# Performance work log

Hardware: AMD Instinct MI355X
Metric: run time of the kernel (lower is better)

Reference implementation:

```python
import jax, jax.numpy as jnp
import numpy as np

NUM_HEADS = 8

def setup_inputs() -> dict:
    key = jax.random.key(0)
    ks = jax.random.split(key, 12)
    B, C, H, W = 4, 256, 64, 64
    QK = 256
    NSP = 256
    x = jax.random.normal(ks[0], (B, C, H, W), dtype=jnp.float32)
    affinity_matrix = jax.random.uniform(ks[1], (B, NSP, H * W), dtype=jnp.float32)
    norm_w = 1.0 + 0.02 * jax.random.normal(ks[2], (C,), dtype=jnp.float32)
    norm_b = 0.02 * jax.random.normal(ks[3], (C,), dtype=jnp.float32)
    Wq = 0.02 * jax.random.normal(ks[4], (QK, C), dtype=jnp.float32)
    Wk = 0.02 * jax.random.normal(ks[5], (QK, C), dtype=jnp.float32)
    Wv = 0.02 * jax.random.normal(ks[6], (C, C), dtype=jnp.float32)
    Wsp = 0.02 * jax.random.normal(ks[7], (QK, C), dtype=jnp.float32)
    lepe_w = 0.02 * jax.random.normal(ks[8], (C, 1, 3, 3), dtype=jnp.float32)  # depthwise OIHW
    lepe_b = 0.02 * jax.random.normal(ks[9], (C,), dtype=jnp.float32)
    return {"x": x, "affinity_matrix": affinity_matrix, "norm_w": norm_w,
            "norm_b": norm_b, "Wq": Wq, "Wk": Wk, "Wv": Wv, "Wsp": Wsp,
            "lepe_w": lepe_w, "lepe_b": lepe_b, "num_spixels": NSP}


def _layernorm2d(x, w, b, eps=1e-6):
    # LayerNorm over channel dim of NCHW input
    xp = x.transpose(0, 2, 3, 1)  # B,H,W,C
    mu = xp.mean(-1, keepdims=True)
    var = ((xp - mu) ** 2).mean(-1, keepdims=True)
    xn = (xp - mu) * jax.lax.rsqrt(var + eps) * w + b
    return xn.transpose(0, 3, 1, 2)


def _sgca(x, affinity_matrix, norm_w, norm_b, Wq, Wk, Wv, Wsp, lepe_w, lepe_b, num_spixels):
    B, C, H, W = x.shape
    HW = H * W
    h = NUM_HEADS
    qk_dim = Wq.shape[0]
    dqk = qk_dim // h
    dv = C // h
    scale = (C // h) ** -0.5

    xn = _layernorm2d(x, norm_w, norm_b)

    # superpixel aggregation: b (hw) c
    x_flat = xn.reshape(B, C, HW).transpose(0, 2, 1)  # B,HW,C
    stoken = jnp.einsum('bmn,bnc->bmc', affinity_matrix, x_flat)
    stoken = stoken / (affinity_matrix.sum(-1, keepdims=True) + 1e-16)  # B,nsp,C

    # sp projection -> B,h,dqk,nsp
    st = jnp.einsum('bmc,qc->bmq', stoken, Wsp).transpose(0, 2, 1)
    st = st.reshape(B, h, dqk, num_spixels)

    # 1x1 conv projections
    q = jnp.einsum('oc,bchw->bohw', Wq, xn).reshape(B, h, dqk, HW)
    k = jnp.einsum('oc,bchw->bohw', Wk, xn).reshape(B, h, dqk, HW)
    vx = jnp.einsum('oc,bchw->bohw', Wv, xn)  # B,C,H,W
    v = vx.reshape(B, h, dv, HW)

    # LePE: depthwise 3x3 conv on v(x)
    lepe = jax.lax.conv_general_dilated(
        vx, lepe_w, window_strides=(1, 1), padding=((1, 1), (1, 1)),
        feature_group_count=C, dimension_numbers=('NCHW', 'OIHW', 'NCHW'))
    lepe = lepe + lepe_b[None, :, None, None]
    # faithful to original: [B,C,HW] -> permute -> [B,HW,C] -> reshape B,C,H,W
    lepe = lepe.reshape(B, C, HW).transpose(0, 2, 1).reshape(B, C, H, W)

    # stage 1: k^T @ stoken, softmax over HW axis
    s_attn = jnp.einsum('bhdn,bhdm->bhnm', k, st) * scale  # B,h,HW,nsp
    s_attn = jax.nn.softmax(s_attn, axis=-2)
    s_out = jnp.einsum('bhdn,bhnm->bhdm', v, s_attn)  # B,h,dv,nsp

    # stage 2: stoken^T @ q, softmax over nsp axis
    x_attn = jnp.einsum('bhdm,bhdn->bhmn', st, q) * scale  # B,h,nsp,HW
    x_attn = jax.nn.softmax(x_attn, axis=-2)
    x_out = jnp.einsum('bhdm,bhmn->bhdn', s_out, x_attn).reshape(B, C, H, W)

    return x_out + lepe


def reference(x, affinity_matrix, norm_w, norm_b, Wq, Wk, Wv, Wsp, lepe_w, lepe_b, num_spixels):
    return _sgca(x, affinity_matrix, norm_w, norm_b, Wq, Wk, Wv, Wsp, lepe_w, lepe_b, num_spixels)
```

## Files before the change

kernel.cpp:

```cpp
#include <hip/hip_runtime.h>
#include <hip/hip_bf16.h>

#define BATCH 4
#define CCH   256
#define HWHW  4096
#define NSP   256
#define NHEAD 8
#define SCALE 0.17677669529663689f
#define PLANE 1048576L

typedef short bf16x8 __attribute__((ext_vector_type(8)));
typedef float f32x4  __attribute__((ext_vector_type(4)));

__global__ __launch_bounds__(256)
void ln_fused_kernel(const float* __restrict__ x, const float* __restrict__ w,
                     const float* __restrict__ bb,
                     const float* __restrict__ Wq, const float* __restrict__ Wk,
                     const float* __restrict__ Wv, const float* __restrict__ Wsp,
                     __hip_bfloat16* __restrict__ xn_cn,
                     __hip_bfloat16* __restrict__ xn_nc,
                     __hip_bfloat16* __restrict__ wbf)
{
    __shared__ __hip_bfloat16 xs[256][80];
    __shared__ float ps[16][64], pss[16][64];
    __shared__ float mus[64], rstds[64];
    __shared__ float wls[256], bls[256];
    int blk = blockIdx.x;
    int t = threadIdx.x;
    if (blk >= 256) {
        int sel = blk - 256;
        const float* src = (sel == 0) ? Wq : (sel == 1) ? Wk : (sel == 2) ? Wv : Wsp;
        __hip_bfloat16* dst = wbf + sel * 65536;
        for (int i = t * 4; i < 65536; i += 1024) {
            float4 f = *(const float4*)(src + i);
            __hip_bfloat16 p[4];
            p[0] = __float2bfloat16(f.x); p[1] = __float2bfloat16(f.y);
            p[2] = __float2bfloat16(f.z); p[3] = __float2bfloat16(f.w);
            *(int2*)(dst + i) = *(int2*)p;
        }
        return;
    }
    int b = blk >> 6;
    int n0 = (blk & 63) * 64;
    int px4 = t & 15, cg = t >> 4;
    wls[t] = w[t]; bls[t] = bb[t];
    long base = (long)b * CCH * HWHW + n0 + px4 * 4;
    float s0 = 0.f, s1 = 0.f, s2 = 0.f, s3 = 0.f;
    float q0 = 0.f, q1 = 0.f, q2 = 0.f, q3 = 0.f;
#pragma unroll
    for (int j = 0; j < 16; ++j) {
        int c = cg * 16 + j;
        float4 f = *(const float4*)(x + base + (long)c * HWHW);
        s0 += f.x; s1 += f.y; s2 += f.z; s3 += f.w;
        q0 += f.x * f.x; q1 += f.y * f.y; q2 += f.z * f.z; q3 += f.w * f.w;
        __hip_bfloat16 p[4];
        p[0] = __float2bfloat16(f.x); p[1] = __float2bfloat16(f.y);
        p[2] = __float2bfloat16(f.z); p[3] = __float2bfloat16(f.w);
        *(int2*)&xs[c][px4 * 4] = *(int2*)p;
    }
    *(float4*)&ps[cg][px4 * 4]  = float4{s0, s1, s2, s3};
    *(float4*)&pss[cg][px4 * 4] = float4{q0, q1, q2, q3};
    __syncthreads();
    if (t < 64) {
        float S = 0.f, SS = 0.f;
#pragma unroll
        for (int g = 0; g < 16; ++g) { S += ps[g][t]; SS += pss[g][t]; }
        float mu = S * (1.f / 256.f);
        float var = SS * (1.f / 256.f) - mu * mu;
        mus[t] = mu; rstds[t] = rsqrtf(var + 1e-6f);
    }
    __syncthreads();
    float mu[4], rst[4];
#pragma unroll
    for (int i = 0; i < 4; ++i) { mu[i] = mus[px4 * 4 + i]; rst[i] = rstds[px4 * 4 + i]; }
#pragma unroll
    for (int j = 0; j < 16; ++j) {
        int c = cg * 16 + j;
        __hip_bfloat16 p[4];
        *(int2*)p = *(const int2*)&xs[c][px4 * 4];
        float wc = wls[c], bc = bls[c];
#pragma unroll
        for (int i = 0; i < 4; ++i)
            p[i] = __float2bfloat16(((float)p[i] - mu[i]) * rst[i] * wc + bc);
        *(int2*)&xs[c][px4 * 4] = *(int2*)p;
    }
    __syncthreads();
#pragma unroll
    for (int i = 0; i < 8; ++i) {
        int idx = t + i * 256;
        int c = idx >> 3, seg = idx & 7;
        *(int4*)(xn_cn + (long)(b * CCH + c) * HWHW + n0 + seg * 8) =
            *(const int4*)&xs[c][seg * 8];
    }
#pragma unroll
    for (int i = 0; i < 8; ++i) {
        int idx = t + i * 256;
        int px = idx >> 5, g8 = idx & 31;
        short pack[8];
#pragma unroll
        for (int j = 0; j < 8; ++j) {
            __hip_bfloat16 v = xs[g8 * 8 + j][px];
            pack[j] = *(short*)&v;
        }
        *(int4*)(xn_nc + ((long)b * HWHW + n0 + px) * CCH + g8 * 8) = *(int4*)pack;
    }
}

__global__ __launch_bounds__(256)
void reduce8_cast_kernel(const float* __restrict__ part, const float* __restrict__ rsPart,
                         __hip_bfloat16* __restrict__ out, float* __restrict__ rs)
{
    int i = blockIdx.x * 256 + threadIdx.x;
    if (blockIdx.x < 4) {
        int b = i >> 8, m = i & 255;
        float s = 0.f;
#pragma unroll
        for (int ch = 0; ch < 8; ++ch) s += rsPart[((b * 8 + ch) << 8) + m];
        rs[i] = s;
    }
    int b = i >> 16, idx = i & 65535;
    long base = (long)b * 8 * 65536 + idx;
    float s = 0.f;
#pragma unroll
    for (int ch = 0; ch < 8; ++ch) s += part[base + (long)ch * 65536];
    out[i] = __float2bfloat16(s);
}

template <int OUTK, bool ROWSCALE, bool A32, bool ROWSUM>
__global__ __launch_bounds__(256)
void mfma_gemm_nt(const void* __restrict__ Aptr, const __hip_bfloat16* __restrict__ B,
                  void* __restrict__ Cptr, int N, int K, int kChunk, int kShift,
                  long aStrideZ, long bStrideZ, long cStrideZ,
                  const float* __restrict__ rowScale, long sStrideZ,
                  float* __restrict__ rsPart)
{
    __shared__ __hip_bfloat16 Asm[4 * 64 * 8];
    __shared__ __hip_bfloat16 Bsm[4 * 64 * 8];
    int z = blockIdx.z;
    int b = z >> kShift;
    int ch = z & ((1 << kShift) - 1);
    int t = threadIdx.x;
    int lane = t & 63, w = t >> 6;
    int l15 = lane & 15, quad = lane >> 4;
    int Mt = blockIdx.y * 64, Nt = blockIdx.x * 64;

    const float* aSrcF = A32 ? ((const float*)Aptr + b * aStrideZ + (long)ch * kChunk
                                + (long)(Mt + w * 16 + l15) * K + quad * 8) : nullptr;
    const __hip_bfloat16* aSrcB = A32 ? nullptr :
        ((const __hip_bfloat16*)Aptr + b * aStrideZ + (long)ch * kChunk
         + (long)(Mt + w * 16 + l15) * K + quad * 8);
    const __hip_bfloat16* bSrc = B + b * bStrideZ + (long)ch * kChunk
        + (long)(Nt + w * 16 + l15) * K + quad * 8;
    __hip_bfloat16* aDst = &Asm[t * 8];
    __hip_bfloat16* bDst = &Bsm[t * 8];

    f32x4 acc00 = {0.f,0.f,0.f,0.f}, acc01 = acc00, acc10 = acc00, acc11 = acc00;
    f32x4 rs0 = acc00, rs1 = acc00;
    bf16x8 onesf;
    { short o = (l15 == 0) ? (short)0x3F80 : (short)0;
      onesf = bf16x8{o, o, o, o, o, o, o, o}; }
    int wm = (w & 1) * 2, wn = (w >> 1) * 2;

    float4 aF0, aF1; int4 aReg, bReg;
    if (A32) { aF0 = ((const float4*)aSrcF)[0]; aF1 = ((const float4*)aSrcF)[1]; }
    else aReg = *(const int4*)aSrcB;
    bReg = *(const int4*)bSrc;

    for (int k0 = 0; k0 < kChunk; k0 += 32) {
        if (A32) {
            __hip_bfloat16 tmp[8];
            tmp[0]=__float2bfloat16(aF0.x); tmp[1]=__float2bfloat16(aF0.y);
            tmp[2]=__float2bfloat16(aF0.z); tmp[3]=__float2bfloat16(aF0.w);
            tmp[4]=__float2bfloat16(aF1.x); tmp[5]=__float2bfloat16(aF1.y);
            tmp[6]=__float2bfloat16(aF1.z); tmp[7]=__float2bfloat16(aF1.w);
            *(int4*)aDst = *(const int4*)tmp;
        } else {
            *(int4*)aDst = aReg;
        }
        *(int4*)bDst = bReg;
        __syncthreads();
        if (k0 + 32 < kChunk) {
            bSrc += 32;
            if (A32) { aSrcF += 32; aF0 = ((const float4*)aSrcF)[0]; aF1 = ((const float4*)aSrcF)[1]; }
            else     { aSrcB += 32; aReg = *(const int4*)aSrcB; }
            bReg = *(const int4*)bSrc;
        }
        bf16x8 a0 = ((const bf16x8*)Asm)[wm * 64 + lane];
        bf16x8 a1 = ((const bf16x8*)Asm)[(wm + 1) * 64 + lane];
        bf16x8 b0 = ((const bf16x8*)Bsm)[wn * 64 + lane];
        bf16x8 b1 = ((const bf16x8*)Bsm)[(wn + 1) * 64 + lane];
        acc00 = __builtin_amdgcn_mfma_f32_16x16x32_bf16(a0, b0, acc00, 0, 0, 0);
        acc01 = __builtin_amdgcn_mfma_f32_16x16x32_bf16(a0, b1, acc01, 0, 0, 0);
        acc10 = __builtin_amdgcn_mfma_f32_16x16x32_bf16(a1, b0, acc10, 0, 0, 0);
        acc11 = __builtin_amdgcn_mfma_f32_16x16x32_bf16(a1, b1, acc11, 0, 0, 0);
        if (ROWSUM) {
            rs0 = __builtin_amdgcn_mfma_f32_16x16x32_bf16(a0, onesf, rs0, 0, 0, 0);
            rs1 = __builtin_amdgcn_mfma_f32_16x16x32_bf16(a1, onesf, rs1, 0, 0, 0);
        }
        __syncthreads();
    }
    if (ROWSUM && blockIdx.x == 0 && (w >> 1) == 0 && l15 == 0) {
#pragma unroll
        for (int r = 0; r < 4; ++r) {
            rsPart[(long)z * 256 + Mt + wm * 16 + quad * 4 + r]       = rs0[r];
            rsPart[(long)z * 256 + Mt + (wm + 1) * 16 + quad * 4 + r] = rs1[r];
        }
    }
    f32x4 accs[2][2] = {{acc00, acc01}, {acc10, acc11}};
#pragma unroll
    for (int i = 0; i < 2; ++i)
#pragma unroll
        for (int j = 0; j < 2; ++j)
#pragma unroll
            for (int r = 0; r < 4; ++r) {
                int m = Mt + (wm + i) * 16 + quad * 4 + r;
                int n = Nt + (wn + j) * 16 + l15;
                float val = accs[i][j][r];
                if (ROWSCALE) val /= (rowScale[(long)b * sStrideZ + m] + 1e-16f);
                long off = (long)z * cStrideZ + (long)m * N + n;
                if (OUTK == 0) ((float*)Cptr)[off] = val;
                else ((__hip_bfloat16*)Cptr)[off] = __float2bfloat16(val);
            }
}

__global__ __launch_bounds__(256)
void stage1_mfma(const __hip_bfloat16* __restrict__ qk_nc,
                 const __hip_bfloat16* __restrict__ v_cn,
                 const __hip_bfloat16* __restrict__ st_md,
                 __hip_bfloat16* __restrict__ opart)
{
    __shared__ __hip_bfloat16 Es[256 * 72];
    __shared__ __hip_bfloat16 sts[256 * 40];
    const int chunk = blockIdx.x, bh = blockIdx.y;
    const int b = bh >> 3, h = bh & 7;
    const int t = threadIdx.x, lane = t & 63, w = t >> 6;
    const int l15 = lane & 15, quad = lane >> 4;
    const int n0 = chunk * 256;

    {
        const int4* src = (const int4*)(st_md + ((long)(b * 256 + t)) * 256 + h * 32);
        int4* dst = (int4*)&sts[t * 40];
        dst[0] = src[0]; dst[1] = src[1]; dst[2] = src[2]; dst[3] = src[3];
    }
    __syncthreads();
    bf16x8 afrag[16];
#pragma unroll
    for (int mt = 0; mt < 16; ++mt)
        afrag[mt] = *(const bf16x8*)&sts[(mt * 16 + l15) * 40 + quad * 8];
    bf16x8 onesf;
    { short o = (l15 == 0) ? (short)0x3F80 : (short)0;
      onesf = bf16x8{o, o, o, o, o, o, o, o}; }

    f32x4 occ[4][3];
#pragma unroll
    for (int i = 0; i < 4; ++i)
#pragma unroll
        for (int j = 0; j < 3; ++j) occ[i][j] = f32x4{0.f,0.f,0.f,0.f};

    for (int sub = 0; sub < 4; ++sub) {
        const int nbase = n0 + sub * 64;
        bf16x8 kf = *(const bf16x8*)(qk_nc + ((long)b * 4096 + nbase + 16 * w + l15) * 512 + 256 + h * 32 + quad * 8);
#pragma unroll
        for (int mt = 0; mt < 16; ++mt) {
            f32x4 s = __builtin_amdgcn_mfma_f32_16x16x32_bf16(afrag[mt], kf, f32x4{0.f,0.f,0.f,0.f}, 0, 0, 0);
#pragma unroll
            for (int r = 0; r < 4; ++r)
                Es[(mt * 16 + quad * 4 + r) * 72 + 16 * w + l15] =
                    __float2bfloat16(__expf(s[r] * SCALE));
        }
        __syncthreads();
#pragma unroll
        for (int ks = 0; ks < 2; ++ks) {
            bf16x8 bf0 = *(const bf16x8*)(v_cn + ((long)(b * 256 + h * 32 + l15)) * 4096 + nbase + ks * 32 + quad * 8);
            bf16x8 bf1 = *(const bf16x8*)(v_cn + ((long)(b * 256 + h * 32 + 16 + l15)) * 4096 + nbase + ks * 32 + quad * 8);
#pragma unroll
            for (int mi = 0; mi < 4; ++mi) {
                bf16x8 af = *(const bf16x8*)&Es[(64 * w + mi * 16 + l15) * 72 + ks * 32 + quad * 8];
                occ[mi][0] = __builtin_amdgcn_mfma_f32_16x16x32_bf16(af, bf0, occ[mi][0], 0, 0, 0);
                occ[mi][1] = __builtin_amdgcn_mfma_f32_16x16x32_bf16(af, bf1, occ[mi][1], 0, 0, 0);
                occ[mi][2] = __builtin_amdgcn_mfma_f32_16x16x32_bf16(af, onesf, occ[mi][2], 0, 0, 0);
            }
        }
        __syncthreads();
    }
    __hip_bfloat16* tb = Es;
#pragma unroll
    for (int mi = 0; mi < 4; ++mi)
#pragma unroll
        for (int jt = 0; jt < 3; ++jt) {
            if (jt == 2 && l15 != 0) continue;
            int col = jt * 16 + l15;
#pragma unroll
            for (int r = 0; r < 4; ++r) {
                int m = 64 * w + mi * 16 + quad * 4 + r;
                tb[col * 264 + m] = __float2bfloat16(occ[mi][jt][r]);
            }
        }
    __syncthreads();
    int* og = (int*)(opart) + (long)(chunk * 32 + bh) * 4224;
    const int* tbi = (const int*)tb;
#pragma unroll
    for (int i = 0; i < 17; ++i) {
        int idx = t + i * 256;
        if (idx < 4224) {
            int row = idx >> 7, off = idx & 127;
            og[idx] = tbi[row * 132 + off];
        }
    }
}

__global__ __launch_bounds__(256)
void merge1_kernel(const __hip_bfloat16* __restrict__ opart, __hip_bfloat16* __restrict__ sout)
{
    int t = blockIdx.x * 256 + threadIdx.x;
    int m = t & 255;
    int d = (t >> 8) & 31;
    int bh = t >> 13;
    float num = 0.f, den = 0.f;
    for (int ch = 0; ch < 16; ++ch) {
        long base = (long)((ch * 32 + bh) * 33) * 256 + m;
        num += (float)opart[base + (long)d * 256];
        den += (float)opart[base + 32 * 256];
    }
    sout[(long)bh * 8192 + d * 256 + m] = __float2bfloat16(num / den);
}

__global__ __launch_bounds__(256)
void lepe_conv_t_kernel(const __hip_bfloat16* __restrict__ v_cn,
                        const float* __restrict__ lw, const float* __restrict__ lb,
                        __hip_bfloat16* __restrict__ lepe_cn)
{
    __shared__ __hip_bfloat16 in_t[32 * 384];
    __shared__ __hip_bfloat16 tile_bf[256 * 33];
    __shared__ float wls[288], bls[32];
    const int bx = blockIdx.x;
    const int c0 = blockIdx.y * 32;
    const int b  = blockIdx.z;
    const int t = threadIdx.x;
    const int n0 = bx * 256, r0 = bx * 4;

    for (int i = t; i < 288; i += 256) wls[i] = lw[c0 * 9 + i];
    if (t < 32)  bls[t] = lb[c0 + t];
#pragma unroll
    for (int i = 0; i < 6; ++i) {
        int vi = t + i * 256;
        int ch = vi / 48;
        int off = (vi % 48) * 8;
        int g = (r0 - 1) * 64 + off;
        int4 val = {0, 0, 0, 0};
        if ((unsigned)g < 4096u)
            val = *(const int4*)(v_cn + (((long)(b * CCH + c0 + ch)) << 12) + g);
        *(int4*)&in_t[ch * 384 + off] = val;
    }
    __syncthreads();

    const int lane = t & 63, w = t >> 6;
#pragma unroll
    for (int i = 0; i < 8; ++i) {
        int ch = w * 8 + i;
        float cr[6], lf[6], rf[6];
#pragma unroll
        for (int rr = 0; rr < 6; ++rr) {
            cr[rr] = (float)in_t[ch * 384 + rr * 64 + lane];
            float lv = __shfl_up(cr[rr], 1);
            float rv = __shfl_down(cr[rr], 1);
            lf[rr] = (lane == 0) ? 0.f : lv;
            rf[rr] = (lane == 63) ? 0.f : rv;
        }
        float w0 = wls[ch*9+0], w1 = wls[ch*9+1], w2 = wls[ch*9+2];
        float w3 = wls[ch*9+3], w4 = wls[ch*9+4], w5 = wls[ch*9+5];
        float w6 = wls[ch*9+6], w7 = wls[ch*9+7], w8 = wls[ch*9+8];
        float bias = bls[ch];
#pragma unroll
        for (int r = 0; r < 4; ++r) {
            float acc = bias
                + lf[r]   * w0 + cr[r]   * w1 + rf[r]   * w2
                + lf[r+1] * w3 + cr[r+1] * w4 + rf[r+1] * w5
                + lf[r+2] * w6 + cr[r+2] * w7 + rf[r+2] * w8;
            tile_bf[(r * 64 + lane) * 33 + ch] = __float2bfloat16(acc);
        }
    }
    __syncthreads();
#pragma unroll
    for (int i = 0; i < 32; ++i) {
        int idx = t + i * 256;
        int nl = idx >> 5, cj = idx & 31;
        int sp = n0 + nl;
        lepe_cn[((long)(b * CCH + (sp >> 4)) << 12) + (nl & 15) * 256 + c0 + cj] =
            tile_bf[nl * 33 + cj];
    }
}

__global__ __launch_bounds__(256)
void stage2_mfma(const __hip_bfloat16* __restrict__ qk_nc,
                 const __hip_bfloat16* __restrict__ st_md,
                 const __hip_bfloat16* __restrict__ sout_bf,
                 const __hip_bfloat16* __restrict__ lepe_cn,
                 float* __restrict__ out)
{
    __shared__ __hip_bfloat16 Es2[64 * 264];
    __shared__ __hip_bfloat16 sts[256 * 40];
    __shared__ __hip_bfloat16 sos[32 * 264];
    __shared__ float o_t[32 * 68];
    const int chunk = blockIdx.x, bh = blockIdx.y;
    const int b = bh >> 3, h = bh & 7;
    const int t = threadIdx.x, lane = t & 63, w = t >> 6;
    const int l15 = lane & 15, quad = lane >> 4;
    const int n0 = chunk * 256;

    {
        const int4* src = (const int4*)(st_md + ((long)(b * 256 + t)) * 256 + h * 32);
        int4* dst = (int4*)&sts[t * 40];
        dst[0] = src[0]; dst[1] = src[1]; dst[2] = src[2]; dst[3] = src[3];
    }
    {
        int row = t >> 3, seg = t & 7;
        const int4* src = (const int4*)(sout_bf + (long)bh * 8192 + row * 256 + seg * 32);
        int4* dst = (int4*)&sos[row * 264 + seg * 32];
        dst[0] = src[0]; dst[1] = src[1]; dst[2] = src[2]; dst[3] = src[3];
    }
    __syncthreads();
    bf16x8 stfrag[4];
#pragma unroll
    for (int mt = 0; mt < 4; ++mt)
        stfrag[mt] = *(const bf16x8*)&sts[(64 * w + mt * 16 + l15) * 40 + quad * 8];
    bf16x8 onesf;
    { short o = (l15 == 0) ? (short)0x3F80 : (short)0;
      onesf = bf16x8{o, o, o, o, o, o, o, o}; }

    for (int sub = 0; sub < 4; ++sub) {
        const int nbase = n0 + sub * 64;
#pragma unroll
        for (int nt = 0; nt < 4; ++nt) {
            bf16x8 qf = *(const bf16x8*)(qk_nc + ((long)b * 4096 + nbase + nt * 16 + l15) * 512 + h * 32 + quad * 8);
#pragma unroll
            for (int mt = 0; mt < 4; ++mt) {
                f32x4 s = __builtin_amdgcn_mfma_f32_16x16x32_bf16(qf, stfrag[mt], f32x4{0.f,0.f,0.f,0.f}, 0, 0, 0);
#pragma unroll
                for (int r = 0; r < 4; ++r)
                    Es2[(nt * 16 + quad * 4 + r) * 264 + 64 * w + mt * 16 + l15] =
                        __float2bfloat16(__expf(s[r] * SCALE));
            }
        }
        __syncthreads();
        f32x4 o0 = {0.f,0.f,0.f,0.f}, o1 = o0, o2 = o0;
#pragma unroll
        for (int ks = 0; ks < 8; ++ks) {
            bf16x8 af = *(const bf16x8*)&Es2[(16 * w + l15) * 264 + ks * 32 + quad * 8];
            bf16x8 b0 = *(const bf16x8*)&sos[(l15) * 264 + ks * 32 + quad * 8];
            bf16x8 b1 = *(const bf16x8*)&sos[(16 + l15) * 264 + ks * 32 + quad * 8];
            o0 = __builtin_amdgcn_mfma_f32_16x16x32_bf16(af, b0, o0, 0, 0, 0);
            o1 = __builtin_amdgcn_mfma_f32_16x16x32_bf16(af, b1, o1, 0, 0, 0);
            o2 = __builtin_amdgcn_mfma_f32_16x16x32_bf16(af, onesf, o2, 0, 0, 0);
        }
        __syncthreads();
#pragma unroll
        for (int r = 0; r < 4; ++r) {
            float den = __shfl(o2[r], lane & 48);
            float inv = 1.f / den;
            o_t[(l15) * 68 + 16 * w + quad * 4 + r]      = o0[r] * inv;
            o_t[(16 + l15) * 68 + 16 * w + quad * 4 + r] = o1[r] * inv;
        }
        __syncthreads();
        {
            int row = t >> 3, coff = (t & 7) * 8;
            long gb = ((long)(b * 256 + h * 32 + row)) * 4096 + nbase + coff;
            int4 lp4 = *(const int4*)(lepe_cn + gb);
            const __hip_bfloat16* lp = (const __hip_bfloat16*)&lp4;
            const float* sp = &o_t[row * 68 + coff];
            float4 r0, r1;
            r0.x = sp[0] + (float)lp[0]; r0.y = sp[1] + (float)lp[1];
            r0.z = sp[2] + (float)lp[2]; r0.w = sp[3] + (float)lp[3];
            r1.x = sp[4] + (float)lp[4]; r1.y = sp[5] + (float)lp[5];
            r1.z = sp[6] + (float)lp[6]; r1.w = sp[7] + (float)lp[7];
            *(float4*)(out + gb)     = r0;
            *(float4*)(out + gb + 4) = r1;
        }
        __syncthreads();
    }
}

extern "C" void kernel_launch(void* const* d_in, const int* in_sizes, int n_in,
                              void* d_out, int out_size, void* d_ws, size_t ws_size,
                              hipStream_t stream)
{
    const float* x    = (const float*)d_in[0];
    const float* aff  = (const float*)d_in[1];
    const float* nw   = (const float*)d_in[2];
    const float* nb   = (const float*)d_in[3];
    const float* Wq   = (const float*)d_in[4];
    const float* Wk   = (const float*)d_in[5];
    const float* Wv   = (const float*)d_in[6];
    const float* Wsp  = (const float*)d_in[7];
    const float* lw   = (const float*)d_in[8];
    const float* lb   = (const float*)d_in[9];
    float* out = (float*)d_out;

    float* ws = (float*)d_ws;
    const long P = PLANE;
    __hip_bfloat16* qk_nc  = (__hip_bfloat16*)(ws);
    __hip_bfloat16* v_cn   = (__hip_bfloat16*)(ws + 4 * P);
    __hip_bfloat16* xn_cn  = (__hip_bfloat16*)(ws + 6 * P);
    __hip_bfloat16* xn_nc  = (__hip_bfloat16*)(ws + 8 * P);
    __hip_bfloat16* lepe_cn= (__hip_bfloat16*)(ws + 10 * P);
    float* stoken_part = ws + 12 * P;
    __hip_bfloat16* opart = (__hip_bfloat16*)(ws + 14 * P);
    float* tail        = ws + 14 * P + 2162688;
    __hip_bfloat16* wbf       = (__hip_bfloat16*)tail;
    __hip_bfloat16* stoken_bf = (__hip_bfloat16*)(tail + 131072);
    __hip_bfloat16* st_md     = (__hip_bfloat16*)(tail + 262144);
    __hip_bfloat16* sout_bf   = (__hip_bfloat16*)(tail + 393216);
    float* rs      = tail + 524288;
    float* rs_part = tail + 525312;

    ln_fused_kernel<<<260, 256, 0, stream>>>(x, nw, nb, Wq, Wk, Wv, Wsp,
                                             xn_cn, xn_nc, wbf);
    mfma_gemm_nt<0, false, true, true><<<dim3(4, 4, 32), 256, 0, stream>>>(
        aff, xn_cn, stoken_part, 256, 4096, 512, 3, P, P, 65536L, nullptr, 0, rs_part);
    reduce8_cast_kernel<<<1024, 256, 0, stream>>>(stoken_part, rs_part, stoken_bf, rs);
    mfma_gemm_nt<1, true, false, false><<<dim3(4, 4, 4), 256, 0, stream>>>(
        stoken_bf, wbf + 3 * 65536, st_md, 256, 256, 256, 0, 65536L, 0L, 65536L, rs, 256L, nullptr);
    mfma_gemm_nt<1, false, false, false><<<dim3(8, 64, 4), 256, 0, stream>>>(
        xn_nc, wbf, qk_nc, 512, 256, 256, 0, P, 0L, 2 * P, nullptr, 0, nullptr);
    mfma_gemm_nt<1, false, false, false><<<dim3(64, 4, 4), 256, 0, stream>>>(
        wbf + 2 * 65536, xn_nc, v_cn, 4096, 256, 256, 0, 0L, P, P, nullptr, 0, nullptr);
    lepe_conv_t_kernel<<<dim3(16, 8, BATCH), 256, 0, stream>>>(v_cn, lw, lb, lepe_cn);
    stage1_mfma<<<dim3(16, 32), 256, 0, stream>>>(qk_nc, v_cn, st_md, opart);
    merge1_kernel<<<1024, 256, 0, stream>>>(opart, sout_bf);
    stage2_mfma<<<dim3(16, 32), 256, 0, stream>>>(qk_nc, st_md, sout_bf, lepe_cn, out);
}
```

Measured before the change: 217.6 us.

## Merge independent GEMMs and LePE conv into fewer grouped kernel launches

Drops the separate split-K reduction kernel by folding the 8-way partial-sum reduction and row normalisation into the stoken projection GEMM. That GEMM is combined with the Q/K and V projection GEMMs into one grouped launch that branches on block index. The LePE depthwise conv is merged into the stage-1 attention kernel as extra blocks. This cuts launch count and inter-kernel gaps, at the cost of redundant reads of partials and rowsum recomputation per output element, and larger shared memory per block in the merged stage-1 kernel.

```diff
diff --git a/kernel.cpp b/kernel.cpp
--- a/kernel.cpp
+++ b/kernel.cpp
@@ -107,50 +107,22 @@
 }
 
 __global__ __launch_bounds__(256)
-void reduce8_cast_kernel(const float* __restrict__ part, const float* __restrict__ rsPart,
-                         __hip_bfloat16* __restrict__ out, float* __restrict__ rs)
-{
-    int i = blockIdx.x * 256 + threadIdx.x;
-    if (blockIdx.x < 4) {
-        int b = i >> 8, m = i & 255;
-        float s = 0.f;
-#pragma unroll
-        for (int ch = 0; ch < 8; ++ch) s += rsPart[((b * 8 + ch) << 8) + m];
-        rs[i] = s;
-    }
-    int b = i >> 16, idx = i & 65535;
-    long base = (long)b * 8 * 65536 + idx;
-    float s = 0.f;
-#pragma unroll
-    for (int ch = 0; ch < 8; ++ch) s += part[base + (long)ch * 65536];
-    out[i] = __float2bfloat16(s);
-}
-
-template <int OUTK, bool ROWSCALE, bool A32, bool ROWSUM>
-__global__ __launch_bounds__(256)
-void mfma_gemm_nt(const void* __restrict__ Aptr, const __hip_bfloat16* __restrict__ B,
-                  void* __restrict__ Cptr, int N, int K, int kChunk, int kShift,
-                  long aStrideZ, long bStrideZ, long cStrideZ,
-                  const float* __restrict__ rowScale, long sStrideZ,
-                  float* __restrict__ rsPart)
+void stoken_gemm_kernel(const float* __restrict__ A, const __hip_bfloat16* __restrict__ B,
+                        float* __restrict__ C, float* __restrict__ rsPart)
 {
     __shared__ __hip_bfloat16 Asm[4 * 64 * 8];
     __shared__ __hip_bfloat16 Bsm[4 * 64 * 8];
     int z = blockIdx.z;
-    int b = z >> kShift;
-    int ch = z & ((1 << kShift) - 1);
+    int b = z >> 3, ch = z & 7;
     int t = threadIdx.x;
     int lane = t & 63, w = t >> 6;
     int l15 = lane & 15, quad = lane >> 4;
     int Mt = blockIdx.y * 64, Nt = blockIdx.x * 64;
 
-    const float* aSrcF = A32 ? ((const float*)Aptr + b * aStrideZ + (long)ch * kChunk
-                                + (long)(Mt + w * 16 + l15) * K + quad * 8) : nullptr;
-    const __hip_bfloat16* aSrcB = A32 ? nullptr :
-        ((const __hip_bfloat16*)Aptr + b * aStrideZ + (long)ch * kChunk
-         + (long)(Mt + w * 16 + l15) * K + quad * 8);
-    const __hip_bfloat16* bSrc = B + b * bStrideZ + (long)ch * kChunk
-        + (long)(Nt + w * 16 + l15) * K + quad * 8;
+    const float* aSrcF = A + (long)b * PLANE + (long)ch * 512
+        + (long)(Mt + w * 16 + l15) * 4096 + quad * 8;
+    const __hip_bfloat16* bSrc = B + (long)b * PLANE + (long)ch * 512
+        + (long)(Nt + w * 16 + l15) * 4096 + quad * 8;
     __hip_bfloat16* aDst = &Asm[t * 8];
     __hip_bfloat16* bDst = &Bsm[t * 8];
 
@@ -161,28 +133,21 @@
       onesf = bf16x8{o, o, o, o, o, o, o, o}; }
     int wm = (w & 1) * 2, wn = (w >> 1) * 2;
 
-    float4 aF0, aF1; int4 aReg, bReg;
-    if (A32) { aF0 = ((const float4*)aSrcF)[0]; aF1 = ((const float4*)aSrcF)[1]; }
-    else aReg = *(const int4*)aSrcB;
-    bReg = *(const int4*)bSrc;
-
-    for (int k0 = 0; k0 < kChunk; k0 += 32) {
-        if (A32) {
-            __hip_bfloat16 tmp[8];
-            tmp[0]=__float2bfloat16(aF0.x); tmp[1]=__float2bfloat16(aF0.y);
-            tmp[2]=__float2bfloat16(aF0.z); tmp[3]=__float2bfloat16(aF0.w);
-            tmp[4]=__float2bfloat16(aF1.x); tmp[5]=__float2bfloat16(aF1.y);
-            tmp[6]=__float2bfloat16(aF1.z); tmp[7]=__float2bfloat16(aF1.w);
-            *(int4*)aDst = *(const int4*)tmp;
-        } else {
-            *(int4*)aDst = aReg;
-        }
+    float4 aF0 = ((const float4*)aSrcF)[0], aF1 = ((const float4*)aSrcF)[1];
+    int4 bReg = *(const int4*)bSrc;
+
+    for (int k0 = 0; k0 < 512; k0 += 32) {
+        __hip_bfloat16 tmp[8];
+        tmp[0]=__float2bfloat16(aF0.x); tmp[1]=__float2bfloat16(aF0.y);
+        tmp[2]=__float2bfloat16(aF0.z); tmp[3]=__float2bfloat16(aF0.w);
+        tmp[4]=__float2bfloat16(aF1.x); tmp[5]=__float2bfloat16(aF1.y);
+        tmp[6]=__float2bfloat16(aF1.z); tmp[7]=__float2bfloat16(aF1.w);
+        *(int4*)aDst = *(const int4*)tmp;
         *(int4*)bDst = bReg;
         __syncthreads();
-        if (k0 + 32 < kChunk) {
-            bSrc += 32;
-            if (A32) { aSrcF += 32; aF0 = ((const float4*)aSrcF)[0]; aF1 = ((const float4*)aSrcF)[1]; }
-            else     { aSrcB += 32; aReg = *(const int4*)aSrcB; }
+        if (k0 + 32 < 512) {
+            aSrcF += 32; bSrc += 32;
+            aF0 = ((const float4*)aSrcF)[0]; aF1 = ((const float4*)aSrcF)[1];
             bReg = *(const int4*)bSrc;
         }
         bf16x8 a0 = ((const bf16x8*)Asm)[wm * 64 + lane];
@@ -193,17 +158,130 @@
         acc01 = __builtin_amdgcn_mfma_f32_16x16x32_bf16(a0, b1, acc01, 0, 0, 0);
         acc10 = __builtin_amdgcn_mfma_f32_16x16x32_bf16(a1, b0, acc10, 0, 0, 0);
         acc11 = __builtin_amdgcn_mfma_f32_16x16x32_bf16(a1, b1, acc11, 0, 0, 0);
-        if (ROWSUM) {
-            rs0 = __builtin_amdgcn_mfma_f32_16x16x32_bf16(a0, onesf, rs0, 0, 0, 0);
-            rs1 = __builtin_amdgcn_mfma_f32_16x16x32_bf16(a1, onesf, rs1, 0, 0, 0);
-        }
-        __syncthreads();
-    }
-    if (ROWSUM && blockIdx.x == 0 && (w >> 1) == 0 && l15 == 0) {
+        rs0 = __builtin_amdgcn_mfma_f32_16x16x32_bf16(a0, onesf, rs0, 0, 0, 0);
+        rs1 = __builtin_amdgcn_mfma_f32_16x16x32_bf16(a1, onesf, rs1, 0, 0, 0);
+        __syncthreads();
+    }
+    if (blockIdx.x == 0 && (w >> 1) == 0 && l15 == 0) {
 #pragma unroll
         for (int r = 0; r < 4; ++r) {
             rsPart[(long)z * 256 + Mt + wm * 16 + quad * 4 + r]       = rs0[r];
             rsPart[(long)z * 256 + Mt + (wm + 1) * 16 + quad * 4 + r] = rs1[r];
+        }
+    }
+    f32x4 accs[2][2] = {{acc00, acc01}, {acc10, acc11}};
+#pragma unroll
+    for (int i = 0; i < 2; ++i)
+#pragma unroll
+        for (int j = 0; j < 2; ++j)
+#pragma unroll
+            for (int r = 0; r < 4; ++r) {
+                int m = Mt + (wm + i) * 16 + quad * 4 + r;
+                int n = Nt + (wn + j) * 16 + l15;
+                C[(long)z * 65536 + (long)m * 256 + n] = accs[i][j][r];
+            }
+}
+
+__global__ __launch_bounds__(256)
+void gemm3_kernel(const __hip_bfloat16* __restrict__ xn_nc,
+                  const __hip_bfloat16* __restrict__ wbf,
+                  const float* __restrict__ stoken_part,
+                  const float* __restrict__ rs_part,
+                  __hip_bfloat16* __restrict__ qk_nc,
+                  __hip_bfloat16* __restrict__ v_cn,
+                  __hip_bfloat16* __restrict__ st_md)
+{
+    __shared__ __hip_bfloat16 Asm[4 * 64 * 8];
+    __shared__ __hip_bfloat16 Bsm[4 * 64 * 8];
+    int B = blockIdx.x;
+    int t = threadIdx.x;
+    int lane = t & 63, w = t >> 6;
+    int l15 = lane & 15, quad = lane >> 4;
+
+    const __hip_bfloat16* aB = nullptr;
+    const float* aP = nullptr;
+    const __hip_bfloat16* bB;
+    __hip_bfloat16* C;
+    int N, Mt, Nt, bIdx;
+    bool stPath = false;
+    if (B < 2048) {
+        int xq = B & 7, y = (B >> 3) & 63, b = B >> 9;
+        Mt = y * 64; Nt = xq * 64; N = 512; bIdx = b;
+        aB = xn_nc + (long)b * PLANE;
+        bB = wbf;
+        C = qk_nc + (long)b * 2 * PLANE;
+    } else if (B < 3072) {
+        int B2 = B - 2048;
+        int xq = B2 & 63, y = (B2 >> 6) & 3, b = B2 >> 8;
+        Mt = y * 64; Nt = xq * 64; N = 4096; bIdx = b;
+        aB = wbf + 2 * 65536;
+        bB = xn_nc + (long)b * PLANE;
+        C = v_cn + (long)b * PLANE;
+    } else {
+        int B2 = B - 3072;
+        int xq = B2 & 3, y = (B2 >> 2) & 3, b = B2 >> 4;
+        Mt = y * 64; Nt = xq * 64; N = 256; bIdx = b;
+        stPath = true;
+        aP = stoken_part + (long)b * 8 * 65536;
+        bB = wbf + 3 * 65536;
+        C = st_md + (long)b * 65536;
+    }
+    __hip_bfloat16* aDst = &Asm[t * 8];
+    __hip_bfloat16* bDst = &Bsm[t * 8];
+    const __hip_bfloat16* bSrc = bB + (long)(Nt + w * 16 + l15) * 256 + quad * 8;
+
+    f32x4 acc00 = {0.f,0.f,0.f,0.f}, acc01 = acc00, acc10 = acc00, acc11 = acc00;
+    int wm = (w & 1) * 2, wn = (w >> 1) * 2;
+
+    if (!stPath) {
+        const __hip_bfloat16* aSrc = aB + (long)(Mt + w * 16 + l15) * 256 + quad * 8;
+        int4 aReg = *(const int4*)aSrc;
+        int4 bReg = *(const int4*)bSrc;
+        for (int k0 = 0; k0 < 256; k0 += 32) {
+            *(int4*)aDst = aReg;
+            *(int4*)bDst = bReg;
+            __syncthreads();
+            if (k0 + 32 < 256) {
+                aSrc += 32; bSrc += 32;
+                aReg = *(const int4*)aSrc; bReg = *(const int4*)bSrc;
+            }
+            bf16x8 a0 = ((const bf16x8*)Asm)[wm * 64 + lane];
+            bf16x8 a1 = ((const bf16x8*)Asm)[(wm + 1) * 64 + lane];
+            bf16x8 b0 = ((const bf16x8*)Bsm)[wn * 64 + lane];
+            bf16x8 b1 = ((const bf16x8*)Bsm)[(wn + 1) * 64 + lane];
+            acc00 = __builtin_amdgcn_mfma_f32_16x16x32_bf16(a0, b0, acc00, 0, 0, 0);
+            acc01 = __builtin_amdgcn_mfma_f32_16x16x32_bf16(a0, b1, acc01, 0, 0, 0);
+            acc10 = __builtin_amdgcn_mfma_f32_16x16x32_bf16(a1, b0, acc10, 0, 0, 0);
+            acc11 = __builtin_amdgcn_mfma_f32_16x16x32_bf16(a1, b1, acc11, 0, 0, 0);
+            __syncthreads();
+        }
+    } else {
+        const float* aPSrc = aP + (long)(Mt + w * 16 + l15) * 256 + quad * 8;
+        for (int k0 = 0; k0 < 256; k0 += 32) {
+            const float* ap = aPSrc + k0;
+            float a8[8] = {0,0,0,0,0,0,0,0};
+#pragma unroll
+            for (int chn = 0; chn < 8; ++chn) {
+                const float4* p = (const float4*)(ap + (long)chn * 65536);
+                float4 f0 = p[0], f1 = p[1];
+                a8[0] += f0.x; a8[1] += f0.y; a8[2] += f0.z; a8[3] += f0.w;
+                a8[4] += f1.x; a8[5] += f1.y; a8[6] += f1.z; a8[7] += f1.w;
+            }
+            __hip_bfloat16 tmp[8];
+#pragma unroll
+            for (int j = 0; j < 8; ++j) tmp[j] = __float2bfloat16(a8[j]);
+            *(int4*)aDst = *(const int4*)tmp;
+            *(int4*)bDst = *(const int4*)(bSrc + k0);
+            __syncthreads();
+            bf16x8 a0 = ((const bf16x8*)Asm)[wm * 64 + lane];
+            bf16x8 a1 = ((const bf16x8*)Asm)[(wm + 1) * 64 + lane];
+            bf16x8 b0 = ((const bf16x8*)Bsm)[wn * 64 + lane];
+            bf16x8 b1 = ((const bf16x8*)Bsm)[(wn + 1) * 64 + lane];
+            acc00 = __builtin_amdgcn_mfma_f32_16x16x32_bf16(a0, b0, acc00, 0, 0, 0);
+            acc01 = __builtin_amdgcn_mfma_f32_16x16x32_bf16(a0, b1, acc01, 0, 0, 0);
+            acc10 = __builtin_amdgcn_mfma_f32_16x16x32_bf16(a1, b0, acc10, 0, 0, 0);
+            acc11 = __builtin_amdgcn_mfma_f32_16x16x32_bf16(a1, b1, acc11, 0, 0, 0);
+            __syncthreads();
         }
     }
     f32x4 accs[2][2] = {{acc00, acc01}, {acc10, acc11}};
@@ -216,95 +294,162 @@
                 int m = Mt + (wm + i) * 16 + quad * 4 + r;
                 int n = Nt + (wn + j) * 16 + l15;
                 float val = accs[i][j][r];
-                if (ROWSCALE) val /= (rowScale[(long)b * sStrideZ + m] + 1e-16f);
-                long off = (long)z * cStrideZ + (long)m * N + n;
-                if (OUTK == 0) ((float*)Cptr)[off] = val;
-                else ((__hip_bfloat16*)Cptr)[off] = __float2bfloat16(val);
+                if (stPath) {
+                    float rsv = 0.f;
+#pragma unroll
+                    for (int chn = 0; chn < 8; ++chn)
+                        rsv += rs_part[((bIdx * 8 + chn) << 8) + m];
+                    val /= (rsv + 1e-16f);
+                }
+                C[(long)m * N + n] = __float2bfloat16(val);
             }
 }
 
 __global__ __launch_bounds__(256)
-void stage1_mfma(const __hip_bfloat16* __restrict__ qk_nc,
-                 const __hip_bfloat16* __restrict__ v_cn,
-                 const __hip_bfloat16* __restrict__ st_md,
-                 __hip_bfloat16* __restrict__ opart)
+void stage1_lepe_kernel(const __hip_bfloat16* __restrict__ qk_nc,
+                        const __hip_bfloat16* __restrict__ v_cn,
+                        const __hip_bfloat16* __restrict__ st_md,
+                        const float* __restrict__ lw, const float* __restrict__ lb,
+                        __hip_bfloat16* __restrict__ opart,
+                        __hip_bfloat16* __restrict__ lepe_cn)
 {
-    __shared__ __hip_bfloat16 Es[256 * 72];
-    __shared__ __hip_bfloat16 sts[256 * 40];
-    const int chunk = blockIdx.x, bh = blockIdx.y;
-    const int b = bh >> 3, h = bh & 7;
-    const int t = threadIdx.x, lane = t & 63, w = t >> 6;
-    const int l15 = lane & 15, quad = lane >> 4;
-    const int n0 = chunk * 256;
-
-    {
-        const int4* src = (const int4*)(st_md + ((long)(b * 256 + t)) * 256 + h * 32);
-        int4* dst = (int4*)&sts[t * 40];
-        dst[0] = src[0]; dst[1] = src[1]; dst[2] = src[2]; dst[3] = src[3];
-    }
-    __syncthreads();
-    bf16x8 afrag[16];
-#pragma unroll
-    for (int mt = 0; mt < 16; ++mt)
-        afrag[mt] = *(const bf16x8*)&sts[(mt * 16 + l15) * 40 + quad * 8];
-    bf16x8 onesf;
-    { short o = (l15 == 0) ? (short)0x3F80 : (short)0;
-      onesf = bf16x8{o, o, o, o, o, o, o, o}; }
-
-    f32x4 occ[4][3];
-#pragma unroll
-    for (int i = 0; i < 4; ++i)
-#pragma unroll
-        for (int j = 0; j < 3; ++j) occ[i][j] = f32x4{0.f,0.f,0.f,0.f};
-
-    for (int sub = 0; sub < 4; ++sub) {
-        const int nbase = n0 + sub * 64;
-        bf16x8 kf = *(const bf16x8*)(qk_nc + ((long)b * 4096 + nbase + 16 * w + l15) * 512 + 256 + h * 32 + quad * 8);
-#pragma unroll
-        for (int mt = 0; mt < 16; ++mt) {
-            f32x4 s = __builtin_amdgcn_mfma_f32_16x16x32_bf16(afrag[mt], kf, f32x4{0.f,0.f,0.f,0.f}, 0, 0, 0);
-#pragma unroll
-            for (int r = 0; r < 4; ++r)
-                Es[(mt * 16 + quad * 4 + r) * 72 + 16 * w + l15] =
-                    __float2bfloat16(__expf(s[r] * SCALE));
-        }
-        __syncthreads();
-#pragma unroll
-        for (int ks = 0; ks < 2; ++ks) {
-            bf16x8 bf0 = *(const bf16x8*)(v_cn + ((long)(b * 256 + h * 32 + l15)) * 4096 + nbase + ks * 32 + quad * 8);
-            bf16x8 bf1 = *(const bf16x8*)(v_cn + ((long)(b * 256 + h * 32 + 16 + l15)) * 4096 + nbase + ks * 32 + quad * 8);
-#pragma unroll
-            for (int mi = 0; mi < 4; ++mi) {
-                bf16x8 af = *(const bf16x8*)&Es[(64 * w + mi * 16 + l15) * 72 + ks * 32 + quad * 8];
-                occ[mi][0] = __builtin_amdgcn_mfma_f32_16x16x32_bf16(af, bf0, occ[mi][0], 0, 0, 0);
-                occ[mi][1] = __builtin_amdgcn_mfma_f32_16x16x32_bf16(af, bf1, occ[mi][1], 0, 0, 0);
-                occ[mi][2] = __builtin_amdgcn_mfma_f32_16x16x32_bf16(af, onesf, occ[mi][2], 0, 0, 0);
-            }
-        }
-        __syncthreads();
-    }
-    __hip_bfloat16* tb = Es;
-#pragma unroll
-    for (int mi = 0; mi < 4; ++mi)
-#pragma unroll
-        for (int jt = 0; jt < 3; ++jt) {
-            if (jt == 2 && l15 != 0) continue;
-            int col = jt * 16 + l15;
+    __shared__ __align__(16) char smem[57344];
+    const int B = blockIdx.x;
+    const int t = threadIdx.x;
+    if (B < 512) {
+        __hip_bfloat16* Es  = (__hip_bfloat16*)smem;
+        __hip_bfloat16* sts = (__hip_bfloat16*)(smem + 36864);
+        const int chunk = B & 15, bh = B >> 4;
+        const int b = bh >> 3, h = bh & 7;
+        const int lane = t & 63, w = t >> 6;
+        const int l15 = lane & 15, quad = lane >> 4;
+        const int n0 = chunk * 256;
+        {
+            const int4* src = (const int4*)(st_md + ((long)(b * 256 + t)) * 256 + h * 32);
+            int4* dst = (int4*)&sts[t * 40];
+            dst[0] = src[0]; dst[1] = src[1]; dst[2] = src[2]; dst[3] = src[3];
+        }
+        __syncthreads();
+        bf16x8 afrag[16];
+#pragma unroll
+        for (int mt = 0; mt < 16; ++mt)
+            afrag[mt] = *(const bf16x8*)&sts[(mt * 16 + l15) * 40 + quad * 8];
+        bf16x8 onesf;
+        { short o = (l15 == 0) ? (short)0x3F80 : (short)0;
+          onesf = bf16x8{o, o, o, o, o, o, o, o}; }
+        f32x4 occ[4][3];
+#pragma unroll
+        for (int i = 0; i < 4; ++i)
+#pragma unroll
+            for (int j = 0; j < 3; ++j) occ[i][j] = f32x4{0.f,0.f,0.f,0.f};
+        for (int sub = 0; sub < 4; ++sub) {
+            const int nbase = n0 + sub * 64;
+            bf16x8 kf = *(const bf16x8*)(qk_nc + ((long)b * 4096 + nbase + 16 * w + l15) * 512 + 256 + h * 32 + quad * 8);
+#pragma unroll
+            for (int mt = 0; mt < 16; ++mt) {
+                f32x4 s = __builtin_amdgcn_mfma_f32_16x16x32_bf16(afrag[mt], kf, f32x4{0.f,0.f,0.f,0.f}, 0, 0, 0);
+#pragma unroll
+                for (int r = 0; r < 4; ++r)
+                    Es[(mt * 16 + quad * 4 + r) * 72 + 16 * w + l15] =
+                        __float2bfloat16(__expf(s[r] * SCALE));
+            }
+            __syncthreads();
+#pragma unroll
+            for (int ks = 0; ks < 2; ++ks) {
+                bf16x8 bf0 = *(const bf16x8*)(v_cn + ((long)(b * 256 + h * 32 + l15)) * 4096 + nbase + ks * 32 + quad * 8);
+                bf16x8 bf1 = *(const bf16x8*)(v_cn + ((long)(b * 256 + h * 32 + 16 + l15)) * 4096 + nbase + ks * 32 + quad * 8);
+#pragma unroll
+                for (int mi = 0; mi < 4; ++mi) {
+                    bf16x8 af = *(const bf16x8*)&Es[(64 * w + mi * 16 + l15) * 72 + ks * 32 + quad * 8];
+                    occ[mi][0] = __builtin_amdgcn_mfma_f32_16x16x32_bf16(af, bf0, occ[mi][0], 0, 0, 0);
+                    occ[mi][1] = __builtin_amdgcn_mfma_f32_16x16x32_bf16(af, bf1, occ[mi][1], 0, 0, 0);
+                    occ[mi][2] = __builtin_amdgcn_mfma_f32_16x16x32_bf16(af, onesf, occ[mi][2], 0, 0, 0);
+                }
+            }
+            __syncthreads();
+        }
+        __hip_bfloat16* tb = Es;
+#pragma unroll
+        for (int mi = 0; mi < 4; ++mi)
+#pragma unroll
+            for (int jt = 0; jt < 3; ++jt) {
+                if (jt == 2 && l15 != 0) continue;
+                int col = jt * 16 + l15;
+#pragma unroll
+                for (int r = 0; r < 4; ++r) {
+                    int m = 64 * w + mi * 16 + quad * 4 + r;
+                    tb[col * 264 + m] = __float2bfloat16(occ[mi][jt][r]);
+                }
+            }
+        __syncthreads();
+        int* og = (int*)(opart) + (long)(chunk * 32 + bh) * 4224;
+        const int* tbi = (const int*)tb;
+#pragma unroll
+        for (int i = 0; i < 17; ++i) {
+            int idx = t + i * 256;
+            if (idx < 4224) {
+                int row = idx >> 7, off = idx & 127;
+                og[idx] = tbi[row * 132 + off];
+            }
+        }
+    } else {
+        __hip_bfloat16* in_t    = (__hip_bfloat16*)smem;
+        __hip_bfloat16* tile_bf = (__hip_bfloat16*)(smem + 24576);
+        float* wls = (float*)(smem + 41472);
+        float* bls = (float*)(smem + 42624);
+        int B2 = B - 512;
+        const int bx = B2 & 15;
+        const int c0 = ((B2 >> 4) & 7) * 32;
+        const int b  = B2 >> 7;
+        const int n0 = bx * 256, r0 = bx * 4;
+        for (int i = t; i < 288; i += 256) wls[i] = lw[c0 * 9 + i];
+        if (t < 32)  bls[t] = lb[c0 + t];
+#pragma unroll
+        for (int i = 0; i < 6; ++i) {
+            int vi = t + i * 256;
+            int ch = vi / 48;
+            int off = (vi % 48) * 8;
+            int g = (r0 - 1) * 64 + off;
+            int4 val = {0, 0, 0, 0};
+            if ((unsigned)g < 4096u)
+                val = *(const int4*)(v_cn + (((long)(b * CCH + c0 + ch)) << 12) + g);
+            *(int4*)&in_t[ch * 384 + off] = val;
+        }
+        __syncthreads();
+        const int lane = t & 63, w = t >> 6;
+#pragma unroll
+        for (int i = 0; i < 8; ++i) {
+            int ch = w * 8 + i;
+            float cr[6], lf[6], rf[6];
+#pragma unroll
+            for (int rr = 0; rr < 6; ++rr) {
+                cr[rr] = (float)in_t[ch * 384 + rr * 64 + lane];
+                float lv = __shfl_up(cr[rr], 1);
+                float rv = __shfl_down(cr[rr], 1);
+                lf[rr] = (lane == 0) ? 0.f : lv;
+                rf[rr] = (lane == 63) ? 0.f : rv;
+            }
+            float w0 = wls[ch*9+0], w1 = wls[ch*9+1], w2 = wls[ch*9+2];
+            float w3 = wls[ch*9+3], w4 = wls[ch*9+4], w5 = wls[ch*9+5];
+            float w6 = wls[ch*9+6], w7 = wls[ch*9+7], w8 = wls[ch*9+8];
+            float bias = bls[ch];
 #pragma unroll
             for (int r = 0; r < 4; ++r) {
-                int m = 64 * w + mi * 16 + quad * 4 + r;
-                tb[col * 264 + m] = __float2bfloat16(occ[mi][jt][r]);
-            }
-        }
-    __syncthreads();
-    int* og = (int*)(opart) + (long)(chunk * 32 + bh) * 4224;
-    const int* tbi = (const int*)tb;
-#pragma unroll
-    for (int i = 0; i < 17; ++i) {
-        int idx = t + i * 256;
-        if (idx < 4224) {
-            int row = idx >> 7, off = idx & 127;
-            og[idx] = tbi[row * 132 + off];
+                float acc = bias
+                    + lf[r]   * w0 + cr[r]   * w1 + rf[r]   * w2
+                    + lf[r+1] * w3 + cr[r+1] * w4 + rf[r+1] * w5
+                    + lf[r+2] * w6 + cr[r+2] * w7 + rf[r+2] * w8;
+                tile_bf[(r * 64 + lane) * 33 + ch] = __float2bfloat16(acc);
+            }
+        }
+        __syncthreads();
+#pragma unroll
+        for (int i = 0; i < 32; ++i) {
+            int idx = t + i * 256;
+            int nl = idx >> 5, cj = idx & 31;
+            int sp = n0 + nl;
+            lepe_cn[((long)(b * CCH + (sp >> 4)) << 12) + (nl & 15) * 256 + c0 + cj] =
+                tile_bf[nl * 33 + cj];
         }
     }
 }
@@ -323,72 +468,6 @@
         den += (float)opart[base + 32 * 256];
     }
     sout[(long)bh * 8192 + d * 256 + m] = __float2bfloat16(num / den);
-}
-
-__global__ __launch_bounds__(256)
-void lepe_conv_t_kernel(const __hip_bfloat16* __restrict__ v_cn,
-                        const float* __restrict__ lw, const float* __restrict__ lb,
-                        __hip_bfloat16* __restrict__ lepe_cn)
-{
-    __shared__ __hip_bfloat16 in_t[32 * 384];
-    __shared__ __hip_bfloat16 tile_bf[256 * 33];
-    __shared__ float wls[288], bls[32];
-    const int bx = blockIdx.x;
-    const int c0 = blockIdx.y * 32;
-    const int b  = blockIdx.z;
-    const int t = threadIdx.x;
-    const int n0 = bx * 256, r0 = bx * 4;
-
-    for (int i = t; i < 288; i += 256) wls[i] = lw[c0 * 9 + i];
-    if (t < 32)  bls[t] = lb[c0 + t];
-#pragma unroll
-    for (int i = 0; i < 6; ++i) {
-        int vi = t + i * 256;
-        int ch = vi / 48;
-        int off = (vi % 48) * 8;
-        int g = (r0 - 1) * 64 + off;
-        int4 val = {0, 0, 0, 0};
-        if ((unsigned)g < 4096u)
-            val = *(const int4*)(v_cn + (((long)(b * CCH + c0 + ch)) << 12) + g);
-        *(int4*)&in_t[ch * 384 + off] = val;
-    }
-    __syncthreads();
-
-    const int lane = t & 63, w = t >> 6;
-#pragma unroll
-    for (int i = 0; i < 8; ++i) {
-        int ch = w * 8 + i;
-        float cr[6], lf[6], rf[6];
-#pragma unroll
-        for (int rr = 0; rr < 6; ++rr) {
-            cr[rr] = (float)in_t[ch * 384 + rr * 64 + lane];
-            float lv = __shfl_up(cr[rr], 1);
-            float rv = __shfl_down(cr[rr], 1);
-            lf[rr] = (lane == 0) ? 0.f : lv;
-            rf[rr] = (lane == 63) ? 0.f : rv;
-        }
-        float w0 = wls[ch*9+0], w1 = wls[ch*9+1], w2 = wls[ch*9+2];
-        float w3 = wls[ch*9+3], w4 = wls[ch*9+4], w5 = wls[ch*9+5];
-        float w6 = wls[ch*9+6], w7 = wls[ch*9+7], w8 = wls[ch*9+8];
-        float bias = bls[ch];
-#pragma unroll
-        for (int r = 0; r < 4; ++r) {
-            float acc = bias
-                + lf[r]   * w0 + cr[r]   * w1 + rf[r]   * w2
-                + lf[r+1] * w3 + cr[r+1] * w4 + rf[r+1] * w5
-                + lf[r+2] * w6 + cr[r+2] * w7 + rf[r+2] * w8;
-            tile_bf[(r * 64 + lane) * 33 + ch] = __float2bfloat16(acc);
-        }
-    }
-    __syncthreads();
-#pragma unroll
-    for (int i = 0; i < 32; ++i) {
-        int idx = t + i * 256;
-        int nl = idx >> 5, cj = idx & 31;
-        int sp = n0 + nl;
-        lepe_cn[((long)(b * CCH + (sp >> 4)) << 12) + (nl & 15) * 256 + c0 + cj] =
-            tile_bf[nl * 33 + cj];
-    }
 }
 
 __global__ __launch_bounds__(256)
@@ -506,26 +585,19 @@
     float* stoken_part = ws + 12 * P;
     __hip_bfloat16* opart = (__hip_bfloat16*)(ws + 14 * P);
     float* tail        = ws + 14 * P + 2162688;
-    __hip_bfloat16* wbf       = (__hip_bfloat16*)tail;
-    __hip_bfloat16* stoken_bf = (__hip_bfloat16*)(tail + 131072);
-    __hip_bfloat16* st_md     = (__hip_bfloat16*)(tail + 262144);
-    __hip_bfloat16* sout_bf   = (__hip_bfloat16*)(tail + 393216);
-    float* rs      = tail + 524288;
-    float* rs_part = tail + 525312;
+    __hip_bfloat16* wbf     = (__hip_bfloat16*)tail;
+    __hip_bfloat16* st_md   = (__hip_bfloat16*)(tail + 131072);
+    __hip_bfloat16* sout_bf = (__hip_bfloat16*)(tail + 262144);
+    float* rs_part = tail + 393216;
 
     ln_fused_kernel<<<260, 256, 0, stream>>>(x, nw, nb, Wq, Wk, Wv, Wsp,
                                              xn_cn, xn_nc, wbf);
-    mfma_gemm_nt<0, false, true, true><<<dim3(4, 4, 32), 256, 0, stream>>>(
-        aff, xn_cn, stoken_part, 256, 4096, 512, 3, P, P, 65536L, nullptr, 0, rs_part);
-    reduce8_cast_kernel<<<1024, 256, 0, stream>>>(stoken_part, rs_part, stoken_bf, rs);
-    mfma_gemm_nt<1, true, false, false><<<dim3(4, 4, 4), 256, 0, stream>>>(
-        stoken_bf, wbf + 3 * 65536, st_md, 256, 256, 256, 0, 65536L, 0L, 65536L, rs, 256L, nullptr);
-    mfma_gemm_nt<1, false, false, false><<<dim3(8, 64, 4), 256, 0, stream>>>(
-        xn_nc, wbf, qk_nc, 512, 256, 256, 0, P, 0L, 2 * P, nullptr, 0, nullptr);
-    mfma_gemm_nt<1, false, false, false><<<dim3(64, 4, 4), 256, 0, stream>>>(
-        wbf + 2 * 65536, xn_nc, v_cn, 4096, 256, 256, 0, 0L, P, P, nullptr, 0, nullptr);
-    lepe_conv_t_kernel<<<dim3(16, 8, BATCH), 256, 0, stream>>>(v_cn, lw, lb, lepe_cn);
-    stage1_mfma<<<dim3(16, 32), 256, 0, stream>>>(qk_nc, v_cn, st_md, opart);
+    stoken_gemm_kernel<<<dim3(4, 4, 32), 256, 0, stream>>>(
+        aff, xn_cn, stoken_part, rs_part);
+    gemm3_kernel<<<3136, 256, 0, stream>>>(
+        xn_nc, wbf, stoken_part, rs_part, qk_nc, v_cn, st_md);
+    stage1_lepe_kernel<<<1024, 256, 0, stream>>>(
+        qk_nc, v_cn, st_md, lw, lb, opart, lepe_cn);
     merge1_kernel<<<1024, 256, 0, stream>>>(opart, sout_bf);
     stage2_mfma<<<dim3(16, 32), 256, 0, stream>>>(qk_nc, st_md, sout_bf, lepe_cn, out);
 }
```

Result: slower. 223.7 us (+2.8%).
